# Kernel tuning notes

Hardware: AMD Instinct MI355X
Metric: run time of the kernel (lower is better)

## Reference

```python
import jax, jax.numpy as jnp
import numpy as np

B = 8192
IN = 2048
H = 2048


def setup_inputs() -> dict:
    key = jax.random.key(0)
    ks = jax.random.split(key, 7)
    s_in = 1.0 / np.sqrt(IN)
    s_h = 1.0 / np.sqrt(H)
    inp = jax.random.normal(ks[0], (B, IN), jnp.float32)
    h0 = jax.random.normal(ks[1], (B, H), jnp.float32)
    c0 = jax.random.normal(ks[2], (B, H), jnp.float32)
    # Packed gate weights: columns ordered [i, f, o, g], each block size H.
    # Equivalent to the 8 separate nn.Linear layers (i_w,f_w,o_w,g_w / i_u,f_u,o_u,g_u).
    W = jax.random.uniform(ks[3], (IN, 4 * H), jnp.float32, -s_in, s_in)
    b_w = jax.random.uniform(ks[4], (4 * H,), jnp.float32, -s_in, s_in)
    U = jax.random.uniform(ks[5], (H, 4 * H), jnp.float32, -s_h, s_h)
    b_u = jax.random.uniform(ks[6], (4 * H,), jnp.float32, -s_h, s_h)
    return {"inp": inp, "h0": h0, "c0": c0, "W": W, "b_w": b_w, "U": U, "b_u": b_u}


def reference(inp, h0, c0, W, b_w, U, b_u):
    # Two big GEMMs instead of eight small ones; identical math.
    gates = inp @ W + b_w + h0 @ U + b_u  # [B, 4H]
    i_g, f_g, o_g, g_g = jnp.split(gates, 4, axis=-1)
    i = jax.nn.sigmoid(i_g)
    f = jax.nn.sigmoid(f_g)
    o = jax.nn.sigmoid(o_g)
    g = jnp.tanh(g_g)
    c = f * c0 + i * g
    h = o * jnp.tanh(c)
    return (h, c)
```

## Files before the change

kernel.cpp:

```cpp
#include <hip/hip_runtime.h>
#include <hip/hip_bf16.h>

#define B_DIM 8192
#define IN_DIM 2048
#define H_DIM 2048
#define K_DIM 4096
#define N4H   8192
#define NT    64

using short8 = __attribute__((ext_vector_type(8))) short;
using f32x4  = __attribute__((ext_vector_type(4))) float;
using u16x4  = __attribute__((ext_vector_type(4))) unsigned short;

__device__ __forceinline__ unsigned short f2bf(float f) {
  union { float f; unsigned int u; } v; v.f = f;
  unsigned int u = v.u;
  return (unsigned short)((u + 0x7FFFu + ((u >> 16) & 1u)) >> 16);
}

__global__ __launch_bounds__(256) void pack_a(const float* __restrict__ inp,
                                              const float* __restrict__ h0,
                                              unsigned short* __restrict__ Ap) {
  size_t idx = ((size_t)blockIdx.x * 256 + threadIdx.x) * 4;
  int b = (int)(idx >> 12);
  int k = (int)(idx & 4095);
  const float* src = (k < IN_DIM) ? (inp + (size_t)b * IN_DIM + k)
                                  : (h0  + (size_t)b * H_DIM + (k - IN_DIM));
  float4 v = *(const float4*)src;
  u16x4 o = { f2bf(v.x), f2bf(v.y), f2bf(v.z), f2bf(v.w) };
  *(u16x4*)&Ap[idx] = o;
}

__global__ __launch_bounds__(256) void pack_b(const float* __restrict__ W,
                                              const float* __restrict__ U,
                                              unsigned short* __restrict__ Bp) {
  __shared__ float tile[64][17];
  const int c0 = blockIdx.x * 16;
  const int k0 = blockIdx.y * 64;
  const int gate  = (c0 >> 4) & 3;
  const int jbase = (c0 >> 6) * 16;
  const int colbase = gate * 2048 + jbase;
  const int t  = threadIdx.x;
  const int cc = t & 15;
  const int r0 = t >> 4;
#pragma unroll
  for (int rr = 0; rr < 4; ++rr) {
    int k = k0 + r0 + rr * 16;
    const float* src = (k < IN_DIM) ? (W + (size_t)k * N4H)
                                    : (U + (size_t)(k - IN_DIM) * N4H);
    tile[r0 + rr * 16][cc] = src[colbase + cc];
  }
  __syncthreads();
  const int c   = t >> 4;
  const int kk0 = (t & 15) * 4;
  u16x4 o = { f2bf(tile[kk0 + 0][c]), f2bf(tile[kk0 + 1][c]),
              f2bf(tile[kk0 + 2][c]), f2bf(tile[kk0 + 3][c]) };
  *(u16x4*)&Bp[(size_t)(c0 + c) * K_DIM + k0 + kk0] = o;
}

__global__ __launch_bounds__(512, 2) void lstm_gemm(
    const unsigned short* __restrict__ Ap,
    const unsigned short* __restrict__ Bp,
    const float* __restrict__ c0,
    const float* __restrict__ b_w,
    const float* __restrict__ b_u,
    float* __restrict__ out) {
  __shared__ unsigned short lds[65536];

  const int t     = threadIdx.x;
  const int lane  = t & 63;
  const int wid   = t >> 6;
  const int wr    = wid >> 2;
  const int wc    = wid & 3;
  const int laneM = lane & 15;
  const int laneG = lane >> 4;

  const int wg  = blockIdx.x;
  const int swz = (wg & 7) * 128 + (wg >> 3);
  const int bm  = swz >> 5;
  const int bn  = swz & 31;

  const int rt   = t >> 3;
  const int gt   = t & 7;
  const int gsw  = gt ^ (rt & 7);
  const unsigned short* gA = Ap + (size_t)(bm * 256 + rt) * K_DIM + gsw * 8;
  const unsigned short* gB = Bp + (size_t)(bn * 256 + rt) * K_DIM + gsw * 8;

#define STAGE(gptr, ldsoff)                                                   \
  __builtin_amdgcn_global_load_lds(                                           \
      (const __attribute__((address_space(1))) void*)(gptr),                  \
      (__attribute__((address_space(3))) void*)&lds[(ldsoff) + t * 8], 16, 0, 0)

#define VMCNT(n) asm volatile("s_waitcnt vmcnt(" #n ")" ::: "memory")
#define BARF()                                                                \
  do {                                                                        \
    asm volatile("" ::: "memory");                                            \
    __builtin_amdgcn_s_barrier();                                             \
    asm volatile("" ::: "memory");                                            \
  } while (0)

  const int sbit = laneM & 7;
  int aoff[2], boff[2];
#pragma unroll
  for (int kk = 0; kk < 2; ++kk) {
    aoff[kk] = wr * 8192 + laneM * 64 + ((kk * 4 + laneG) ^ sbit) * 8;
    boff[kk] = 16384 + (wc >> 1) * 8192 + ((wc & 1) * 64 + laneM) * 64
               + ((kk * 4 + laneG) ^ sbit) * 8;
  }

#define RD_AF(AF, BASE, PH)                                                   \
  _Pragma("unroll")                                                           \
  for (int i = 0; i < 2; ++i)                                                 \
    _Pragma("unroll")                                                         \
    for (int kk = 0; kk < 2; ++kk)                                            \
      AF[i][kk] = *(const short8*)&lds[(BASE) + aoff[kk] + (2 * (PH) + i) * 1024];

#define RD_BF(BASE)                                                           \
  _Pragma("unroll")                                                           \
  for (int n = 0; n < 4; ++n)                                                 \
    _Pragma("unroll")                                                         \
    for (int kk = 0; kk < 2; ++kk)                                            \
      bfr[n][kk] = *(const short8*)&lds[(BASE) + boff[kk] + n * 1024];

#define MFMA16(Q, AF)                                                         \
  __builtin_amdgcn_s_setprio(1);                                              \
  _Pragma("unroll")                                                           \
  for (int i = 0; i < 2; ++i)                                                 \
    _Pragma("unroll")                                                         \
    for (int n = 0; n < 4; ++n)                                               \
      _Pragma("unroll")                                                       \
      for (int kk = 0; kk < 2; ++kk)                                          \
        acc[2 * (Q) + i][n] = __builtin_amdgcn_mfma_f32_16x16x32_bf16(        \
            AF[i][kk], bfr[n][kk], acc[2 * (Q) + i][n], 0, 0, 0);             \
  __builtin_amdgcn_s_setprio(0)

  f32x4 acc[8][4];
#pragma unroll
  for (int m = 0; m < 8; ++m)
#pragma unroll
    for (int n = 0; n < 4; ++n)
      acc[m][n] = (f32x4){0.f, 0.f, 0.f, 0.f};

  short8 af0[2][2], af1[2][2], bfr[4][2];

  const int j = (bn * 4 + wc) * 16 + laneM;
  float bias[4];
#pragma unroll
  for (int g = 0; g < 4; ++g)
    bias[g] = b_w[g * 2048 + j] + b_u[g * 2048 + j];
  asm volatile("s_waitcnt vmcnt(0)" ::: "memory");

  STAGE(gA,               0);
  STAGE(gA + 128 * K_DIM, 8192);
  STAGE(gB,               16384);
  STAGE(gB +  64 * K_DIM, 16384 + 4096);
  STAGE(gB + 128 * K_DIM, 16384 + 8192);
  STAGE(gB + 192 * K_DIM, 16384 + 12288);
  STAGE(gA +  64 * K_DIM, 4096);
  STAGE(gA + 192 * K_DIM, 12288);
  VMCNT(2);
  BARF();
  RD_AF(af0, 0, 0);
  RD_BF(0);

#pragma unroll 1
  for (int kt = 0; kt < NT - 1; ++kt) {
    const int cb = (kt & 1) << 15;
    const int db = cb ^ 32768;
    const unsigned short* gA1 = gA + (kt + 1) * 64;
    const unsigned short* gB1 = gB + (kt + 1) * 64;
    STAGE(gA1,               db + 0);
    STAGE(gA1 + 128 * K_DIM, db + 8192);
    BARF();
    RD_AF(af1, cb, 1);
    MFMA16(0, af0);
    STAGE(gB1,               db + 16384);
    STAGE(gB1 +  64 * K_DIM, db + 16384 + 4096);
    VMCNT(4);
    BARF();
    RD_AF(af0, cb, 2);
    MFMA16(1, af1);
    STAGE(gB1 + 128 * K_DIM, db + 16384 + 8192);
    STAGE(gB1 + 192 * K_DIM, db + 16384 + 12288);
    BARF();
    RD_AF(af1, cb, 3);
    MFMA16(2, af0);
    STAGE(gA1 +  64 * K_DIM, db + 4096);
    STAGE(gA1 + 192 * K_DIM, db + 12288);
    VMCNT(2);
    BARF();
    RD_AF(af0, db, 0);
    MFMA16(3, af1);
    RD_BF(db);
  }

  {
    RD_AF(af1, 32768, 1);
    MFMA16(0, af0);
    VMCNT(0);
    BARF();
    RD_AF(af0, 32768, 2);
    MFMA16(1, af1);
    RD_AF(af1, 32768, 3);
    MFMA16(2, af0);
    MFMA16(3, af1);
  }

  const int rbase = bm * 256 + wr * 128 + laneG * 4;
  float* outH = out;
  float* outC = out + (size_t)B_DIM * H_DIM;
#pragma unroll
  for (int m = 0; m < 8; ++m) {
#pragma unroll
    for (int r = 0; r < 4; ++r) {
      const int bi = rbase + m * 16 + r;
      const size_t off = (size_t)bi * H_DIM + j;
      float ig = acc[m][0][r] + bias[0];
      float fg = acc[m][1][r] + bias[1];
      float og = acc[m][2][r] + bias[2];
      float gg = acc[m][3][r] + bias[3];
      float iv = 1.f / (1.f + __expf(-ig));
      float fv = 1.f / (1.f + __expf(-fg));
      float ov = 1.f / (1.f + __expf(-og));
      float gv = 2.f / (1.f + __expf(-2.f * gg)) - 1.f;
      float cv = fv * c0[off] + iv * gv;
      float tc = 2.f / (1.f + __expf(-2.f * cv)) - 1.f;
      outH[off] = ov * tc;
      outC[off] = cv;
    }
  }
}

extern "C" void kernel_launch(void* const* d_in, const int* in_sizes, int n_in,
                              void* d_out, int out_size, void* d_ws, size_t ws_size,
                              hipStream_t stream) {
  const float* inp = (const float*)d_in[0];
  const float* h0  = (const float*)d_in[1];
  const float* c0  = (const float*)d_in[2];
  const float* W   = (const float*)d_in[3];
  const float* b_w = (const float*)d_in[4];
  const float* U   = (const float*)d_in[5];
  const float* b_u = (const float*)d_in[6];
  float* out = (float*)d_out;

  unsigned short* Ap = (unsigned short*)d_ws;
  unsigned short* Bp = Ap + (size_t)B_DIM * K_DIM;

  pack_a<<<(B_DIM * K_DIM / 4) / 256, 256, 0, stream>>>(inp, h0, Ap);
  dim3 gb(N4H / 16, K_DIM / 64);
  pack_b<<<gb, 256, 0, stream>>>(W, U, Bp);
  lstm_gemm<<<1024, 512, 0, stream>>>(Ap, Bp, c0, b_w, b_u, out);
}
```

Measured before the change: 565.3 us.

## Switch LSTM GEMM to 32x32x16 MFMA with 4x2 wave layout

Replaces the 16x16x32 bf16 MFMA tiling with 32x32x16 MFMA. The 8 waves are rearranged into a 4x2 grid with 64x128 tiles per wave, and the B packing is rewritten so each 32-column block holds all four gates. The LDS read schedule is restructured into four k-substeps, each with its own A and B fragment loads, and a full vmcnt(0) wait before each tile swap. The larger MFMA shape is meant to cut LDS fragment traffic and instruction count, at the cost of a less staggered global-load/compute overlap.

```diff
diff --git a/kernel.cpp b/kernel.cpp
--- a/kernel.cpp
+++ b/kernel.cpp
@@ -9,7 +9,7 @@
 #define NT    64
 
 using short8 = __attribute__((ext_vector_type(8))) short;
-using f32x4  = __attribute__((ext_vector_type(4))) float;
+using f32x16 = __attribute__((ext_vector_type(16))) float;
 using u16x4  = __attribute__((ext_vector_type(4))) unsigned short;
 
 __device__ __forceinline__ unsigned short f2bf(float f) {
@@ -37,9 +37,8 @@
   __shared__ float tile[64][17];
   const int c0 = blockIdx.x * 16;
   const int k0 = blockIdx.y * 64;
-  const int gate  = (c0 >> 4) & 3;
-  const int jbase = (c0 >> 6) * 16;
-  const int colbase = gate * 2048 + jbase;
+  const int gate    = (c0 >> 5) & 3;
+  const int colbase = gate * 2048 + (c0 >> 7) * 32 + (c0 & 16);
   const int t  = threadIdx.x;
   const int cc = t & 15;
   const int r0 = t >> 4;
@@ -67,13 +66,13 @@
     float* __restrict__ out) {
   __shared__ unsigned short lds[65536];
 
-  const int t     = threadIdx.x;
-  const int lane  = t & 63;
-  const int wid   = t >> 6;
-  const int wr    = wid >> 2;
-  const int wc    = wid & 3;
-  const int laneM = lane & 15;
-  const int laneG = lane >> 4;
+  const int t    = threadIdx.x;
+  const int lane = t & 63;
+  const int wid  = t >> 6;
+  const int wr   = wid >> 1;
+  const int wc   = wid & 1;
+  const int l31  = lane & 31;
+  const int lhi  = lane >> 5;
 
   const int wg  = blockIdx.x;
   const int swz = (wg & 7) * 128 + (wg >> 3);
@@ -99,69 +98,65 @@
     asm volatile("" ::: "memory");                                            \
   } while (0)
 
-  const int sbit = laneM & 7;
-  int aoff[2], boff[2];
-#pragma unroll
-  for (int kk = 0; kk < 2; ++kk) {
-    aoff[kk] = wr * 8192 + laneM * 64 + ((kk * 4 + laneG) ^ sbit) * 8;
-    boff[kk] = 16384 + (wc >> 1) * 8192 + ((wc & 1) * 64 + laneM) * 64
-               + ((kk * 4 + laneG) ^ sbit) * 8;
-  }
-
-#define RD_AF(AF, BASE, PH)                                                   \
-  _Pragma("unroll")                                                           \
-  for (int i = 0; i < 2; ++i)                                                 \
+  const int s = l31 & 7;
+  int abase[2], bbase[4], koff[4];
+#pragma unroll
+  for (int mf = 0; mf < 2; ++mf)
+    abase[mf] = wr * 4096 + (mf * 32 + l31) * 64;
+#pragma unroll
+  for (int nf = 0; nf < 4; ++nf)
+    bbase[nf] = 16384 + (wc * 128 + nf * 32 + l31) * 64;
+#pragma unroll
+  for (int kk = 0; kk < 4; ++kk)
+    koff[kk] = ((2 * kk + lhi) ^ s) * 8;
+
+#define RD_K(AF, BF, BASE, KK)                                                \
+  do {                                                                        \
     _Pragma("unroll")                                                         \
-    for (int kk = 0; kk < 2; ++kk)                                            \
-      AF[i][kk] = *(const short8*)&lds[(BASE) + aoff[kk] + (2 * (PH) + i) * 1024];
-
-#define RD_BF(BASE)                                                           \
-  _Pragma("unroll")                                                           \
-  for (int n = 0; n < 4; ++n)                                                 \
+    for (int mf = 0; mf < 2; ++mf)                                            \
+      AF[mf] = *(const short8*)&lds[(BASE) + abase[mf] + koff[KK]];           \
     _Pragma("unroll")                                                         \
-    for (int kk = 0; kk < 2; ++kk)                                            \
-      bfr[n][kk] = *(const short8*)&lds[(BASE) + boff[kk] + n * 1024];
-
-#define MFMA16(Q, AF)                                                         \
+    for (int nf = 0; nf < 4; ++nf)                                            \
+      BF[nf] = *(const short8*)&lds[(BASE) + bbase[nf] + koff[KK]];           \
+  } while (0)
+
+#define MFMA8(AF, BF)                                                         \
   __builtin_amdgcn_s_setprio(1);                                              \
   _Pragma("unroll")                                                           \
-  for (int i = 0; i < 2; ++i)                                                 \
+  for (int mf = 0; mf < 2; ++mf)                                              \
     _Pragma("unroll")                                                         \
-    for (int n = 0; n < 4; ++n)                                               \
-      _Pragma("unroll")                                                       \
-      for (int kk = 0; kk < 2; ++kk)                                          \
-        acc[2 * (Q) + i][n] = __builtin_amdgcn_mfma_f32_16x16x32_bf16(        \
-            AF[i][kk], bfr[n][kk], acc[2 * (Q) + i][n], 0, 0, 0);             \
+    for (int nf = 0; nf < 4; ++nf)                                            \
+      acc[mf][nf] = __builtin_amdgcn_mfma_f32_32x32x16_bf16(                  \
+          AF[mf], BF[nf], acc[mf][nf], 0, 0, 0);                              \
   __builtin_amdgcn_s_setprio(0)
 
-  f32x4 acc[8][4];
-#pragma unroll
-  for (int m = 0; m < 8; ++m)
-#pragma unroll
-    for (int n = 0; n < 4; ++n)
-      acc[m][n] = (f32x4){0.f, 0.f, 0.f, 0.f};
-
-  short8 af0[2][2], af1[2][2], bfr[4][2];
-
-  const int j = (bn * 4 + wc) * 16 + laneM;
+  f32x16 acc[2][4];
+#pragma unroll
+  for (int mf = 0; mf < 2; ++mf)
+#pragma unroll
+    for (int nf = 0; nf < 4; ++nf)
+      acc[mf][nf] = (f32x16)(0.f);
+
+  short8 af0[2], af1[2], bf0[4], bf1[4];
+
+  const int j = (bn * 2 + wc) * 32 + l31;
   float bias[4];
 #pragma unroll
   for (int g = 0; g < 4; ++g)
     bias[g] = b_w[g * 2048 + j] + b_u[g * 2048 + j];
   asm volatile("s_waitcnt vmcnt(0)" ::: "memory");
 
-  STAGE(gA,               0);
-  STAGE(gA + 128 * K_DIM, 8192);
   STAGE(gB,               16384);
   STAGE(gB +  64 * K_DIM, 16384 + 4096);
   STAGE(gB + 128 * K_DIM, 16384 + 8192);
   STAGE(gB + 192 * K_DIM, 16384 + 12288);
+  STAGE(gA,               0);
   STAGE(gA +  64 * K_DIM, 4096);
+  STAGE(gA + 128 * K_DIM, 8192);
   STAGE(gA + 192 * K_DIM, 12288);
-  VMCNT(2);
+  VMCNT(0);
   BARF();
-  RD_AF(af0, 0, 0);
-  RD_BF(0);
+  RD_K(af0, bf0, 0, 0);
 
 #pragma unroll 1
   for (int kt = 0; kt < NT - 1; ++kt) {
@@ -169,56 +164,51 @@
     const int db = cb ^ 32768;
     const unsigned short* gA1 = gA + (kt + 1) * 64;
     const unsigned short* gB1 = gB + (kt + 1) * 64;
-    STAGE(gA1,               db + 0);
-    STAGE(gA1 + 128 * K_DIM, db + 8192);
-    BARF();
-    RD_AF(af1, cb, 1);
-    MFMA16(0, af0);
     STAGE(gB1,               db + 16384);
     STAGE(gB1 +  64 * K_DIM, db + 16384 + 4096);
-    VMCNT(4);
-    BARF();
-    RD_AF(af0, cb, 2);
-    MFMA16(1, af1);
+    BARF();
+    RD_K(af1, bf1, cb, 1);
+    MFMA8(af0, bf0);
     STAGE(gB1 + 128 * K_DIM, db + 16384 + 8192);
     STAGE(gB1 + 192 * K_DIM, db + 16384 + 12288);
     BARF();
-    RD_AF(af1, cb, 3);
-    MFMA16(2, af0);
+    RD_K(af0, bf0, cb, 2);
+    MFMA8(af1, bf1);
+    STAGE(gA1,               db + 0);
     STAGE(gA1 +  64 * K_DIM, db + 4096);
+    STAGE(gA1 + 128 * K_DIM, db + 8192);
     STAGE(gA1 + 192 * K_DIM, db + 12288);
-    VMCNT(2);
-    BARF();
-    RD_AF(af0, db, 0);
-    MFMA16(3, af1);
-    RD_BF(db);
+    BARF();
+    RD_K(af1, bf1, cb, 3);
+    MFMA8(af0, bf0);
+    VMCNT(0);
+    BARF();
+    RD_K(af0, bf0, db, 0);
+    MFMA8(af1, bf1);
   }
 
   {
-    RD_AF(af1, 32768, 1);
-    MFMA16(0, af0);
-    VMCNT(0);
-    BARF();
-    RD_AF(af0, 32768, 2);
-    MFMA16(1, af1);
-    RD_AF(af1, 32768, 3);
-    MFMA16(2, af0);
-    MFMA16(3, af1);
-  }
-
-  const int rbase = bm * 256 + wr * 128 + laneG * 4;
+    RD_K(af1, bf1, 32768, 1);
+    MFMA8(af0, bf0);
+    RD_K(af0, bf0, 32768, 2);
+    MFMA8(af1, bf1);
+    RD_K(af1, bf1, 32768, 3);
+    MFMA8(af0, bf0);
+    MFMA8(af1, bf1);
+  }
+
   float* outH = out;
   float* outC = out + (size_t)B_DIM * H_DIM;
 #pragma unroll
-  for (int m = 0; m < 8; ++m) {
-#pragma unroll
-    for (int r = 0; r < 4; ++r) {
-      const int bi = rbase + m * 16 + r;
+  for (int mf = 0; mf < 2; ++mf) {
+#pragma unroll
+    for (int reg = 0; reg < 16; ++reg) {
+      const int bi = bm * 256 + wr * 64 + mf * 32 + (reg & 3) + 8 * (reg >> 2) + 4 * lhi;
       const size_t off = (size_t)bi * H_DIM + j;
-      float ig = acc[m][0][r] + bias[0];
-      float fg = acc[m][1][r] + bias[1];
-      float og = acc[m][2][r] + bias[2];
-      float gg = acc[m][3][r] + bias[3];
+      float ig = acc[mf][0][reg] + bias[0];
+      float fg = acc[mf][1][reg] + bias[1];
+      float og = acc[mf][2][reg] + bias[2];
+      float gg = acc[mf][3][reg] + bias[3];
       float iv = 1.f / (1.f + __expf(-ig));
       float fv = 1.f / (1.f + __expf(-fg));
       float ov = 1.f / (1.f + __expf(-og));
```

Result: slower. 698.7 us (+23.6%).
